# Kernel optimization log

Measured on AMD Instinct MI355X. Metric: run time of the kernel, lower is better.

The kernel has to match this reference:

```python
import jax, jax.numpy as jnp
import numpy as np

N_STEPS = 8          # spatial_interval
SPATIAL_SCALE = 1.0  # spatial_scale


def setup_inputs() -> dict:
    key = jax.random.key(0)
    ks = jax.random.split(key, 6)
    B, N, D = 32, 1024, 256
    x = jax.random.normal(ks[0], (B, N, D), dtype=jnp.float32)
    adj_mx = jax.random.uniform(ks[1], (N, N), dtype=jnp.float32) / N  # row-scaled dense adjacency
    alpha_train = jnp.ones((N,), dtype=jnp.float32)          # alpha * ones(num_node), alpha=1.0
    w = jnp.eye(D, dtype=jnp.float32) + 0.01 * jax.random.normal(ks[2], (D, D), dtype=jnp.float32)
    d = jax.random.uniform(ks[3], (D,), dtype=jnp.float32)
    fc_in_w = jax.random.normal(ks[4], (D, D), dtype=jnp.float32) * (1.0 / np.sqrt(D))
    fc_in_b = jnp.zeros((D,), dtype=jnp.float32)
    return {"x": x, "adj_mx": adj_mx, "alpha_train": alpha_train, "w": w,
            "d": d, "fc_in_w": fc_in_w, "fc_in_b": fc_in_b, "vt": 0}


def reference(x, adj_mx, alpha_train, w, d, fc_in_w, fc_in_b, vt):
    # x: [B, N, D]. x0 is detached in torch (x.clone().detach()).
    x0 = jax.lax.stop_gradient(x)
    # fc_in (dropout is identity in eval mode)
    h = jnp.einsum('bnd,ed->bne', x, fc_in_w) + fc_in_b
    # constants of the diffusion ODE
    alph = jax.nn.sigmoid(alpha_train)[:, None]          # [N, 1]
    d_clamped = jnp.clip(d, 0.0, 1.0)
    w_eff = (w * d_clamped) @ w.T                        # [D, D]
    dt = jnp.float32(SPATIAL_SCALE / N_STEPS)

    def euler_step(h, _):
        ax = jnp.einsum('nm,bmd->bnd', adj_mx, h)        # graph diffusion
        f = alph * 0.5 * (ax - h) + h @ w_eff - h + x0
        return h + dt * f, None

    h, _ = jax.lax.scan(euler_step, h, None, length=N_STEPS)
    return h
```

## Files before the change

### kernel.cpp

```cpp
#include <hip/hip_runtime.h>
#include <hip/hip_bf16.h>
#include <stdint.h>

typedef __bf16 bf16;
typedef __bf16 bf16x8 __attribute__((ext_vector_type(8)));
typedef __bf16 bf16x4 __attribute__((ext_vector_type(4)));
typedef float f32x4 __attribute__((ext_vector_type(4)));
typedef unsigned short u16;

__device__ __forceinline__ void gload_lds16(const bf16* g, bf16* l) {
    __builtin_amdgcn_global_load_lds(
        (const __attribute__((address_space(1))) void*)g,
        (__attribute__((address_space(3))) void*)l, 16, 0, 0);
}

template <int LD>
__device__ __forceinline__ void stage(const bf16* __restrict__ g, bf16* l, int t) {
    int sw = ((t & 7) ^ ((t >> 3) & 7)) << 3;
    size_t base = (size_t)(t >> 3) * LD + sw;
#pragma unroll
    for (int k = 0; k < 4; ++k)
        gload_lds16(g + base + (size_t)(k * 32) * LD, l + t * 8 + k * 2048);
}

#define LDSW(buf, row, kc) \
    (*(const bf16x8*)&(buf)[(row) * 64 + ((((kc) ^ ((row) & 7))) << 3)])

__global__ void prep_alpha(const float* __restrict__ a, float* __restrict__ out) {
    int i = blockIdx.x * blockDim.x + threadIdx.x;
    if (i < 1024) out[i] = 0.5f / (1.0f + __expf(-a[i]));
}

__global__ void prep_adj(const float* __restrict__ adj, const float* __restrict__ ahs,
                         bf16* __restrict__ adjb) {
    int i = blockIdx.x * blockDim.x + threadIdx.x;
    int row = i >> 8;
    float s = ahs[row];
    float4 v = ((const float4*)adj)[i];
    bf16x4 o = {(bf16)(s * v.x), (bf16)(s * v.y), (bf16)(s * v.z), (bf16)(s * v.w)};
    ((bf16x4*)adjb)[i] = o;
}

__global__ void cast_f32_bf16x4(const float* __restrict__ src, bf16* __restrict__ dst,
                                int n4) {
    int i = blockIdx.x * blockDim.x + threadIdx.x;
    if (i < n4) {
        float4 v = ((const float4*)src)[i];
        bf16x4 o = {(bf16)v.x, (bf16)v.y, (bf16)v.z, (bf16)v.w};
        ((bf16x4*)dst)[i] = o;
    }
}

__global__ void prep_weff(const float* __restrict__ w, const float* __restrict__ dv,
                          bf16* __restrict__ weffT) {
    __shared__ float wk[256];
    __shared__ float dd[256];
    int k = blockIdx.x, j = threadIdx.x;
    dd[j] = fminf(fmaxf(dv[j], 0.0f), 1.0f);
    wk[j] = w[k * 256 + j];
    __syncthreads();
    float s = 0.0f;
#pragma unroll 8
    for (int c = 0; c < 256; ++c) s += wk[c] * dd[c] * w[j * 256 + c];
    weffT[j * 256 + k] = (bf16)s;
}

__global__ void prep_xT(const float* __restrict__ x, bf16* __restrict__ xT,
                        bf16* __restrict__ xb) {
    __shared__ bf16 tile[64][65];
    int b = blockIdx.z, n0 = blockIdx.x * 64, d0 = blockIdx.y * 64;
    int t = threadIdx.x;
    int i = t >> 4, j4 = (t & 15) * 4;
#pragma unroll
    for (int p = 0; p < 4; ++p) {
        int n = i + p * 16;
        size_t gi = (((size_t)b << 10) + n0 + n) * 256 + d0 + j4;
        float4 v = *(const float4*)&x[gi];
        bf16x4 o = {(bf16)v.x, (bf16)v.y, (bf16)v.z, (bf16)v.w};
        *(bf16x4*)&xb[gi] = o;
        tile[n][j4 + 0] = o[0]; tile[n][j4 + 1] = o[1];
        tile[n][j4 + 2] = o[2]; tile[n][j4 + 3] = o[3];
    }
    __syncthreads();
#pragma unroll
    for (int p = 0; p < 4; ++p) {
        int c = p * 256 + t;
        int d = c >> 4, nc = c & 15;
        bf16x4 o = {tile[nc * 4 + 0][d], tile[nc * 4 + 1][d],
                    tile[nc * 4 + 2][d], tile[nc * 4 + 3][d]};
        *(bf16x4*)&xT[(((size_t)(b * 256 + d0 + d)) << 10) + n0 + nc * 4] = o;
    }
}

__device__ __forceinline__ void stChunk(const bf16* __restrict__ g, int ld,
                                        bf16* l, int c) {
    int row = c >> 3, slot = c & 7;
    gload_lds16(g + (size_t)row * ld + ((slot ^ (row & 7)) << 3), l + c * 8);
}
__device__ __forceinline__ void stageA4(const bf16* __restrict__ g, int lda,
                                        bf16* l, int t) {
#pragma unroll
    for (int i = 0; i < 4; ++i) stChunk(g, lda, l, (i << 8) + t);
}
__device__ __forceinline__ void stageB2(const bf16* __restrict__ g, int ldb,
                                        bf16* l, int t) {
#pragma unroll
    for (int i = 0; i < 2; ++i) stChunk(g, ldb, l, (i << 8) + t);
}

__device__ __forceinline__ void mma_tile(const bf16* A, const bf16* B,
                                         f32x4 acc[2][4], int lane, int wv) {
    const int r0 = wv * 32 + (lane & 15);
    const int kq = lane >> 4;
    bf16x8 a[2][2], b[4][2];
#pragma unroll
    for (int mi = 0; mi < 2; ++mi) {
        int rA = r0 + mi * 16;
#pragma unroll
        for (int kk = 0; kk < 2; ++kk) a[mi][kk] = LDSW(A, rA, kk * 4 + kq);
    }
#pragma unroll
    for (int ni = 0; ni < 4; ++ni) {
        int rB = ni * 16 + (lane & 15);
#pragma unroll
        for (int kk = 0; kk < 2; ++kk) b[ni][kk] = LDSW(B, rB, kk * 4 + kq);
    }
#pragma unroll
    for (int kk = 0; kk < 2; ++kk)
#pragma unroll
        for (int mi = 0; mi < 2; ++mi)
#pragma unroll
            for (int ni = 0; ni < 4; ++ni)
                acc[mi][ni] = __builtin_amdgcn_mfma_f32_16x16x32_bf16(
                    a[mi][kk], b[ni][kk], acc[mi][ni], 0, 0, 0);
}

template <int NT, typename F>
__device__ __forceinline__ void run_pipeline(F tadr, bf16 (*As)[8192],
                                             bf16 (*Bs)[4096], f32x4 acc[2][4],
                                             int t, int lane, int wv) {
    {
        const bf16 *Ag, *Bg; int lda, ldb;
        tadr(0, Ag, lda, Bg, ldb);
        stageA4(Ag, lda, As[0], t);
        stageB2(Bg, ldb, Bs[0], t);
        if (NT > 1) {
            tadr(1, Ag, lda, Bg, ldb);
            stageA4(Ag, lda, As[1], t);
            stageB2(Bg, ldb, Bs[1], t);
        }
    }
    int cur = 0, pre = 2;
#pragma unroll 1
    for (int i = 0; i < NT; ++i) {
        if (i + 2 < NT) {
            const bf16 *Ag, *Bg; int lda, ldb;
            tadr(i + 2, Ag, lda, Bg, ldb);
            stageA4(Ag, lda, As[pre], t);
            stageB2(Bg, ldb, Bs[pre], t);
            asm volatile("s_waitcnt vmcnt(12)" ::: "memory");
        } else if (i + 1 < NT) {
            asm volatile("s_waitcnt vmcnt(6)" ::: "memory");
        } else {
            asm volatile("s_waitcnt vmcnt(0)" ::: "memory");
        }
        __builtin_amdgcn_s_barrier();
        mma_tile(As[cur], Bs[cur], acc, lane, wv);
        __builtin_amdgcn_s_barrier();
        cur = (cur == 2) ? 0 : cur + 1;
        pre = (pre == 2) ? 0 : pre + 1;
    }
}

__launch_bounds__(256, 2)
__global__ void gemm_fcin(const bf16* __restrict__ xb, const bf16* __restrict__ fcwb,
                          const float* __restrict__ fcb,
                          bf16* __restrict__ hb, bf16* __restrict__ hT,
                          bf16* __restrict__ hloT) {
    __shared__ __align__(16) bf16 As[3][8192];
    __shared__ __align__(16) bf16 Bs[3][4096];
    int t = threadIdx.x, lane = t & 63, wv = t >> 6;
    int row0 = blockIdx.y * 128;
    int col0 = blockIdx.x * 64;
    f32x4 acc[2][4] = {};
    const bf16* Ab = xb + (size_t)row0 * 256;
    const bf16* Bb = fcwb + (size_t)col0 * 256;
    auto tadr = [&](int i, const bf16*& Ag, int& lda, const bf16*& Bg, int& ldb) {
        Ag = Ab + i * 64; lda = 256;
        Bg = Bb + i * 64; ldb = 256;
    };
    run_pipeline<4>(tadr, As, Bs, acc, t, lane, wv);

    int rbase = row0 + wv * 32 + ((lane >> 4) << 2);
    int cbase = col0 + (lane & 15);
#pragma unroll
    for (int mi = 0; mi < 2; ++mi) {
        int rg = rbase + mi * 16;
#pragma unroll
        for (int ni = 0; ni < 4; ++ni) {
            int col = cbase + ni * 16;
            float bias = fcb[col];
            bf16x4 tv, lv;
#pragma unroll
            for (int r = 0; r < 4; ++r) {
                float v = acc[mi][ni][r] + bias;
                size_t idx = (size_t)(rg + r) * 256 + col;
                bf16 hi = (bf16)v;
                hb[idx] = hi;
                tv[r] = hi;
                lv[r] = (bf16)(v - (float)hi);
            }
            int b = rg >> 10, n = rg & 1023;
            size_t tb = (((size_t)(b * 256 + col)) << 10) + n;
            *(bf16x4*)&hT[tb] = tv;
            *(bf16x4*)&hloT[tb] = lv;
        }
    }
}

template <bool LAST>
__launch_bounds__(256, 2)
__global__ void gemm_step(const bf16* __restrict__ adjb, const bf16* __restrict__ hbp,
                          const bf16* __restrict__ hTp, const bf16* __restrict__ weffT,
                          const float* __restrict__ ahs, const bf16* __restrict__ xT,
                          bf16* __restrict__ hloT, bf16* __restrict__ hbn,
                          bf16* __restrict__ hTn, float* __restrict__ out) {
    __shared__ __align__(16) char smem[65536];
    bf16 (*As)[8192] = (bf16(*)[8192])smem;
    bf16 (*Bs)[8192] = (bf16(*)[8192])(smem + 32768);
    int t = threadIdx.x, lane = t & 63, wv = t >> 6;
    int wm = wv >> 1, wn = wv & 1;
    int g = blockIdx.x;
    int xcd = g & 7, rest = g >> 3;
    int b = (rest & 3) * 8 + xcd;
    int tile = rest >> 2;
    int n0 = (tile & 7) * 128;
    int d0 = (tile >> 3) * 128;
    f32x4 acc[4][4] = {};

    const bf16* A1 = adjb + (size_t)n0 * 1024;
    const bf16* B1 = hTp + ((size_t)(b * 256 + d0)) * 1024;
    const bf16* A2 = hbp + ((size_t)(b * 1024 + n0)) * 256;
    const bf16* B2 = weffT + (size_t)d0 * 256;

    const int l15 = lane & 15, kq = lane >> 4;
    int rA[4], rB[4];
#pragma unroll
    for (int j = 0; j < 4; ++j) {
        rA[j] = wm * 64 + j * 16 + l15;
        rB[j] = wn * 64 + j * 16 + l15;
    }

    stage<1024>(A1, As[0], t);
    stage<1024>(B1, Bs[0], t);

#pragma unroll 1
    for (int i = 0; i < 20; ++i) {
        asm volatile("s_waitcnt vmcnt(0)" ::: "memory");
        __builtin_amdgcn_s_barrier();
        if (i + 1 < 20) {
            if (i + 1 < 16) {
                stage<1024>(A1 + (i + 1) * 64, As[(i + 1) & 1], t);
                stage<1024>(B1 + (i + 1) * 64, Bs[(i + 1) & 1], t);
            } else {
                stage<256>(A2 + (i - 15) * 64, As[(i + 1) & 1], t);
                stage<256>(B2 + (i - 15) * 64, Bs[(i + 1) & 1], t);
            }
        }
        const bf16* A = As[i & 1];
        const bf16* B = Bs[i & 1];
#pragma unroll
        for (int kk = 0; kk < 2; ++kk) {
            int kc = kk * 4 + kq;
            bf16x8 a[4], bfr[4];
#pragma unroll
            for (int j = 0; j < 4; ++j) bfr[j] = LDSW(B, rB[j], kc);
#pragma unroll
            for (int j = 0; j < 4; ++j) a[j] = LDSW(A, rA[j], kc);
#pragma unroll
            for (int mi = 0; mi < 4; ++mi)
#pragma unroll
                for (int ni = 0; ni < 4; ++ni)
                    acc[mi][ni] = __builtin_amdgcn_mfma_f32_16x16x32_bf16(
                        a[mi], bfr[ni], acc[mi][ni], 0, 0, 0);
        }
    }
    __builtin_amdgcn_s_barrier();

    const float dt = 0.125f;
    const int lq = (lane >> 4) << 2;
    bf16* img = (bf16*)smem;
    const int PADN = 132;
#pragma unroll
    for (int mi = 0; mi < 4; ++mi) {
        int nl = wm * 64 + mi * 16 + lq;
        int ng = n0 + nl;
        f32x4 av = *(const f32x4*)&ahs[ng];
#pragma unroll
        for (int ni = 0; ni < 4; ++ni) {
            int cl = wn * 64 + ni * 16 + l15;
            int cg = d0 + cl;
            size_t tb = (((size_t)(b * 256 + cg)) << 10) + ng;
            bf16x4 hp = *(const bf16x4*)&hTp[tb];
            bf16x4 lp = *(const bf16x4*)&hloT[tb];
            bf16x4 xp = *(const bf16x4*)&xT[tb];
            bf16x4 nhi, nlo;
#pragma unroll
            for (int r = 0; r < 4; ++r) {
                float hold = (float)hp[r] + (float)lp[r];
                float f = acc[mi][ni][r] - (av[r] + 1.0f) * hold + (float)xp[r];
                float hv = hold + dt * f;
                if (LAST) {
                    out[(((size_t)b << 10) + ng + r) * 256 + cg] = hv;
                } else {
                    bf16 hi2 = (bf16)hv;
                    nhi[r] = hi2;
                    nlo[r] = (bf16)(hv - (float)hi2);
                }
            }
            if (!LAST) {
                *(bf16x4*)&hTn[tb] = nhi;
                *(bf16x4*)&hloT[tb] = nlo;
                int nsw = nl ^ (((cl >> 3) & 7) << 2);
                *(bf16x4*)&img[cl * PADN + nsw] = nhi;
            }
        }
    }
    if (!LAST) {
        asm volatile("s_waitcnt lgkmcnt(0)" ::: "memory");
        __builtin_amdgcn_s_barrier();
        const u16* imgu = (const u16*)img;
#pragma unroll
        for (int P = 0; P < 8; ++P) {
            int chunk = P * 256 + t;
            int node = chunk >> 4;
            int c8 = chunk & 15;
            u16 v[8];
#pragma unroll
            for (int k = 0; k < 8; ++k) {
                int col = c8 * 8 + k;
                v[k] = imgu[col * PADN + (node ^ (((col >> 3) & 7) << 2))];
            }
            uint4 pk;
            pk.x = v[0] | ((unsigned)v[1] << 16);
            pk.y = v[2] | ((unsigned)v[3] << 16);
            pk.z = v[4] | ((unsigned)v[5] << 16);
            pk.w = v[6] | ((unsigned)v[7] << 16);
            *(uint4*)&hbn[(((size_t)b << 10) + n0 + node) * 256 + d0 + c8 * 8] = pk;
        }
    }
}

extern "C" void kernel_launch(void* const* d_in, const int* in_sizes, int n_in,
                              void* d_out, int out_size, void* d_ws, size_t ws_size,
                              hipStream_t stream) {
    const float* x     = (const float*)d_in[0];
    const float* adj   = (const float*)d_in[1];
    const float* alpha = (const float*)d_in[2];
    const float* w     = (const float*)d_in[3];
    const float* dvec  = (const float*)d_in[4];
    const float* fcw   = (const float*)d_in[5];
    const float* fcb   = (const float*)d_in[6];
    float* out = (float*)d_out;

    const size_t HB = (size_t)32 * 1024 * 256 * 2;
    char* p = (char*)d_ws;
    bf16* hb0   = (bf16*)p; p += HB;
    bf16* hb1   = (bf16*)p; p += HB;
    bf16* hT0   = (bf16*)p; p += HB;
    bf16* hT1   = (bf16*)p; p += HB;
    bf16* xb    = (bf16*)p; p += HB;
    bf16* hloT  = (bf16*)p; p += HB;
    bf16* xT    = (bf16*)p; p += HB;
    bf16* adjb  = (bf16*)p; p += (size_t)1024 * 1024 * 2;
    bf16* fcwb  = (bf16*)p; p += 256 * 256 * 2;
    bf16* weffT = (bf16*)p; p += 256 * 256 * 2;
    float* ahs  = (float*)p; p += 1024 * 4;

    prep_alpha<<<4, 256, 0, stream>>>(alpha, ahs);
    prep_adj<<<1024, 256, 0, stream>>>(adj, ahs, adjb);
    prep_weff<<<256, 256, 0, stream>>>(w, dvec, weffT);
    prep_xT<<<dim3(16, 4, 32), 256, 0, stream>>>(x, xT, xb);
    cast_f32_bf16x4<<<64, 256, 0, stream>>>(fcw, fcwb, 16384);

    gemm_fcin<<<dim3(4, 256), 256, 0, stream>>>(xb, fcwb, fcb, hb0, hT0, hloT);

    bf16* hb[2] = {hb0, hb1};
    bf16* hT[2] = {hT0, hT1};
    int cur = 0;
    for (int s = 0; s < 8; ++s) {
        if (s < 7)
            gemm_step<false><<<512, 256, 0, stream>>>(
                adjb, hb[cur], hT[cur], weffT, ahs, xT, hloT,
                hb[cur ^ 1], hT[cur ^ 1], out);
        else
            gemm_step<true><<<512, 256, 0, stream>>>(
                adjb, hb[cur], hT[cur], weffT, ahs, xT, hloT,
                hb[cur ^ 1], hT[cur ^ 1], out);
        cur ^= 1;
    }
}
```

Before: 381.3 us.

## Drop row-major h copy; read transposed h for the w_eff GEMM phase

Removes the row-major bf16 copy of h that was produced through an LDS transpose in every step's epilogue and in fc_in. The h@w_eff phase now stages tiles from the transposed hT buffer and builds A fragments with scalar strided LDS reads. This cuts global writes and the epilogue transpose pass. The cost is slower, possibly bank-conflicted element-wise LDS fragment loads for the last 4 K-tiles.

```diff
diff --git a/kernel.cpp b/kernel.cpp
--- a/kernel.cpp
+++ b/kernel.cpp
@@ -21,6 +21,15 @@
 #pragma unroll
     for (int k = 0; k < 4; ++k)
         gload_lds16(g + base + (size_t)(k * 32) * LD, l + t * 8 + k * 2048);
+}
+
+__device__ __forceinline__ void stageT2(const bf16* __restrict__ g, bf16* l, int t) {
+#pragma unroll
+    for (int k = 0; k < 4; ++k) {
+        int ch = k * 256 + t;
+        int c = ch >> 4, n8 = ch & 15;
+        gload_lds16(g + ((size_t)c << 10) + n8 * 8, l + ch * 8);
+    }
 }
 
 #define LDSW(buf, row, kc) \
@@ -175,8 +184,7 @@
 __launch_bounds__(256, 2)
 __global__ void gemm_fcin(const bf16* __restrict__ xb, const bf16* __restrict__ fcwb,
                           const float* __restrict__ fcb,
-                          bf16* __restrict__ hb, bf16* __restrict__ hT,
-                          bf16* __restrict__ hloT) {
+                          bf16* __restrict__ hT, bf16* __restrict__ hloT) {
     __shared__ __align__(16) bf16 As[3][8192];
     __shared__ __align__(16) bf16 Bs[3][4096];
     int t = threadIdx.x, lane = t & 63, wv = t >> 6;
@@ -204,9 +212,7 @@
 #pragma unroll
             for (int r = 0; r < 4; ++r) {
                 float v = acc[mi][ni][r] + bias;
-                size_t idx = (size_t)(rg + r) * 256 + col;
                 bf16 hi = (bf16)v;
-                hb[idx] = hi;
                 tv[r] = hi;
                 lv[r] = (bf16)(v - (float)hi);
             }
@@ -220,11 +226,11 @@
 
 template <bool LAST>
 __launch_bounds__(256, 2)
-__global__ void gemm_step(const bf16* __restrict__ adjb, const bf16* __restrict__ hbp,
+__global__ void gemm_step(const bf16* __restrict__ adjb,
                           const bf16* __restrict__ hTp, const bf16* __restrict__ weffT,
                           const float* __restrict__ ahs, const bf16* __restrict__ xT,
-                          bf16* __restrict__ hloT, bf16* __restrict__ hbn,
-                          bf16* __restrict__ hTn, float* __restrict__ out) {
+                          bf16* __restrict__ hloT, bf16* __restrict__ hTn,
+                          float* __restrict__ out) {
     __shared__ __align__(16) char smem[65536];
     bf16 (*As)[8192] = (bf16(*)[8192])smem;
     bf16 (*Bs)[8192] = (bf16(*)[8192])(smem + 32768);
@@ -240,7 +246,7 @@
 
     const bf16* A1 = adjb + (size_t)n0 * 1024;
     const bf16* B1 = hTp + ((size_t)(b * 256 + d0)) * 1024;
-    const bf16* A2 = hbp + ((size_t)(b * 1024 + n0)) * 256;
+    const bf16* T2 = hTp + (((size_t)(b * 256)) << 10) + n0;
     const bf16* B2 = weffT + (size_t)d0 * 256;
 
     const int l15 = lane & 15, kq = lane >> 4;
@@ -263,43 +269,60 @@
                 stage<1024>(A1 + (i + 1) * 64, As[(i + 1) & 1], t);
                 stage<1024>(B1 + (i + 1) * 64, Bs[(i + 1) & 1], t);
             } else {
-                stage<256>(A2 + (i - 15) * 64, As[(i + 1) & 1], t);
-                stage<256>(B2 + (i - 15) * 64, Bs[(i + 1) & 1], t);
+                stageT2(T2 + ((size_t)((i + 1 - 16) * 64) << 10), As[(i + 1) & 1], t);
+                stage<256>(B2 + (i + 1 - 16) * 64, Bs[(i + 1) & 1], t);
             }
         }
         const bf16* A = As[i & 1];
         const bf16* B = Bs[i & 1];
-#pragma unroll
-        for (int kk = 0; kk < 2; ++kk) {
-            int kc = kk * 4 + kq;
-            bf16x8 a[4], bfr[4];
-#pragma unroll
-            for (int j = 0; j < 4; ++j) bfr[j] = LDSW(B, rB[j], kc);
-#pragma unroll
-            for (int j = 0; j < 4; ++j) a[j] = LDSW(A, rA[j], kc);
-#pragma unroll
-            for (int mi = 0; mi < 4; ++mi)
-#pragma unroll
-                for (int ni = 0; ni < 4; ++ni)
-                    acc[mi][ni] = __builtin_amdgcn_mfma_f32_16x16x32_bf16(
-                        a[mi], bfr[ni], acc[mi][ni], 0, 0, 0);
-        }
-    }
-    __builtin_amdgcn_s_barrier();
+        if (i < 16) {
+#pragma unroll
+            for (int kk = 0; kk < 2; ++kk) {
+                int kc = kk * 4 + kq;
+                bf16x8 a[4], bfr[4];
+#pragma unroll
+                for (int j = 0; j < 4; ++j) bfr[j] = LDSW(B, rB[j], kc);
+#pragma unroll
+                for (int j = 0; j < 4; ++j) a[j] = LDSW(A, rA[j], kc);
+#pragma unroll
+                for (int mi = 0; mi < 4; ++mi)
+#pragma unroll
+                    for (int ni = 0; ni < 4; ++ni)
+                        acc[mi][ni] = __builtin_amdgcn_mfma_f32_16x16x32_bf16(
+                            a[mi], bfr[ni], acc[mi][ni], 0, 0, 0);
+            }
+        } else {
+#pragma unroll
+            for (int kk = 0; kk < 2; ++kk) {
+                int kc = kk * 4 + kq;
+                bf16x8 a[4], bfr[4];
+#pragma unroll
+                for (int j = 0; j < 4; ++j) bfr[j] = LDSW(B, rB[j], kc);
+                int crow = kq * 8 + kk * 32;
+#pragma unroll
+                for (int j = 0; j < 4; ++j)
+#pragma unroll
+                    for (int e = 0; e < 8; ++e)
+                        a[j][e] = A[(crow + e) * 128 + rA[j]];
+#pragma unroll
+                for (int mi = 0; mi < 4; ++mi)
+#pragma unroll
+                    for (int ni = 0; ni < 4; ++ni)
+                        acc[mi][ni] = __builtin_amdgcn_mfma_f32_16x16x32_bf16(
+                            a[mi], bfr[ni], acc[mi][ni], 0, 0, 0);
+            }
+        }
+    }
 
     const float dt = 0.125f;
     const int lq = (lane >> 4) << 2;
-    bf16* img = (bf16*)smem;
-    const int PADN = 132;
 #pragma unroll
     for (int mi = 0; mi < 4; ++mi) {
-        int nl = wm * 64 + mi * 16 + lq;
-        int ng = n0 + nl;
+        int ng = n0 + wm * 64 + mi * 16 + lq;
         f32x4 av = *(const f32x4*)&ahs[ng];
 #pragma unroll
         for (int ni = 0; ni < 4; ++ni) {
-            int cl = wn * 64 + ni * 16 + l15;
-            int cg = d0 + cl;
+            int cg = d0 + wn * 64 + ni * 16 + l15;
             size_t tb = (((size_t)(b * 256 + cg)) << 10) + ng;
             bf16x4 hp = *(const bf16x4*)&hTp[tb];
             bf16x4 lp = *(const bf16x4*)&hloT[tb];
@@ -321,32 +344,7 @@
             if (!LAST) {
                 *(bf16x4*)&hTn[tb] = nhi;
                 *(bf16x4*)&hloT[tb] = nlo;
-                int nsw = nl ^ (((cl >> 3) & 7) << 2);
-                *(bf16x4*)&img[cl * PADN + nsw] = nhi;
-            }
-        }
-    }
-    if (!LAST) {
-        asm volatile("s_waitcnt lgkmcnt(0)" ::: "memory");
-        __builtin_amdgcn_s_barrier();
-        const u16* imgu = (const u16*)img;
-#pragma unroll
-        for (int P = 0; P < 8; ++P) {
-            int chunk = P * 256 + t;
-            int node = chunk >> 4;
-            int c8 = chunk & 15;
-            u16 v[8];
-#pragma unroll
-            for (int k = 0; k < 8; ++k) {
-                int col = c8 * 8 + k;
-                v[k] = imgu[col * PADN + (node ^ (((col >> 3) & 7) << 2))];
-            }
-            uint4 pk;
-            pk.x = v[0] | ((unsigned)v[1] << 16);
-            pk.y = v[2] | ((unsigned)v[3] << 16);
-            pk.z = v[4] | ((unsigned)v[5] << 16);
-            pk.w = v[6] | ((unsigned)v[7] << 16);
-            *(uint4*)&hbn[(((size_t)b << 10) + n0 + node) * 256 + d0 + c8 * 8] = pk;
+            }
         }
     }
 }
@@ -365,8 +363,6 @@
 
     const size_t HB = (size_t)32 * 1024 * 256 * 2;
     char* p = (char*)d_ws;
-    bf16* hb0   = (bf16*)p; p += HB;
-    bf16* hb1   = (bf16*)p; p += HB;
     bf16* hT0   = (bf16*)p; p += HB;
     bf16* hT1   = (bf16*)p; p += HB;
     bf16* xb    = (bf16*)p; p += HB;
@@ -383,20 +379,17 @@
     prep_xT<<<dim3(16, 4, 32), 256, 0, stream>>>(x, xT, xb);
     cast_f32_bf16x4<<<64, 256, 0, stream>>>(fcw, fcwb, 16384);
 
-    gemm_fcin<<<dim3(4, 256), 256, 0, stream>>>(xb, fcwb, fcb, hb0, hT0, hloT);
-
-    bf16* hb[2] = {hb0, hb1};
+    gemm_fcin<<<dim3(4, 256), 256, 0, stream>>>(xb, fcwb, fcb, hT0, hloT);
+
     bf16* hT[2] = {hT0, hT1};
     int cur = 0;
     for (int s = 0; s < 8; ++s) {
         if (s < 7)
             gemm_step<false><<<512, 256, 0, stream>>>(
-                adjb, hb[cur], hT[cur], weffT, ahs, xT, hloT,
-                hb[cur ^ 1], hT[cur ^ 1], out);
+                adjb, hT[cur], weffT, ahs, xT, hloT, hT[cur ^ 1], out);
         else
             gemm_step<true><<<512, 256, 0, stream>>>(
-                adjb, hb[cur], hT[cur], weffT, ahs, xT, hloT,
-                hb[cur ^ 1], hT[cur ^ 1], out);
+                adjb, hT[cur], weffT, ahs, xT, hloT, hT[cur ^ 1], out);
         cur ^= 1;
     }
 }
```

Measured after the change: 387.7 us. Within noise of the previous version (+1.7%).
